# Kernel optimization log

Hardware: AMD Instinct MI355X
Metric: run time of the kernel (lower is better)

## Reference

```python
import jax, jax.numpy as jnp
import numpy as np

B, H, W, C = 1, 72, 72, 768
NH, HD = 12, 64
FF = 3072
EPS = 1e-6
THETA = 10000.0
S = H * W


def _rope_tables():
    freqs = 1.0 / THETA ** (np.arange(0, HD, 4, dtype=np.float32) / HD)  # [16]
    t = np.arange(H, dtype=np.float32)
    fx = np.outer(t, freqs)  # [72,16]
    fy = np.outer(t, freqs)
    fx = np.tile(fx[:, None, :], (1, W, 1))  # [72,72,16]
    fy = np.tile(fy[None, :, :], (H, 1, 1))
    fxy = np.concatenate([fx, fy], axis=-1).reshape(S, -1)  # [5184,32]
    fxy = np.repeat(fxy, 2, axis=-1)  # [5184,64]
    return jnp.asarray(np.cos(fxy)), jnp.asarray(np.sin(fxy))


def _rotate_pairwise(x):
    x1 = x[..., ::2]
    x2 = x[..., 1::2]
    return jnp.stack([-x2, x1], axis=-1).reshape(x.shape)


def _layernorm(x, g, b):
    m = jnp.mean(x, axis=-1, keepdims=True)
    v = jnp.mean(jnp.square(x - m), axis=-1, keepdims=True)
    return (x - m) * jax.lax.rsqrt(v + EPS) * g + b


def setup_inputs() -> dict:
    key = jax.random.key(0)
    ks = jax.random.split(key, 12)
    s_c = 1.0 / np.sqrt(C)
    s_ff = 1.0 / np.sqrt(FF)
    d = {
        "hidden_states": jax.random.normal(ks[0], (B, H, W, C), jnp.float32),
        "wq": jax.random.normal(ks[1], (C, C), jnp.float32) * s_c,
        "bq": jnp.zeros((C,), jnp.float32),
        "wk": jax.random.normal(ks[2], (C, C), jnp.float32) * s_c,
        "bk": jnp.zeros((C,), jnp.float32),
        "wv": jax.random.normal(ks[3], (C, C), jnp.float32) * s_c,
        "bv": jnp.zeros((C,), jnp.float32),
        "wo": jax.random.normal(ks[4], (C, C), jnp.float32) * s_c,
        "bo": jnp.zeros((C,), jnp.float32),
        "g1": jnp.ones((C,), jnp.float32),
        "b1": jnp.zeros((C,), jnp.float32),
        "g2": jnp.ones((C,), jnp.float32),
        "b2": jnp.zeros((C,), jnp.float32),
        "w_fc1": jax.random.normal(ks[5], (C, FF), jnp.float32) * s_c,
        "b_fc1": jnp.zeros((FF,), jnp.float32),
        "w_fc2": jax.random.normal(ks[6], (FF, C), jnp.float32) * s_ff,
        "b_fc2": jnp.zeros((C,), jnp.float32),
        "ls1": jnp.full((C,), 1e-5, jnp.float32),
        "ls2": jnp.full((C,), 1e-5, jnp.float32),
    }
    return d


def reference(hidden_states, wq, bq, wk, bk, wv, bv, wo, bo, g1, b1, g2, b2,
              w_fc1, b_fc1, w_fc2, b_fc2, ls1, ls2):
    cos, sin = _rope_tables()  # [S, HD]
    cos = cos[None, None]  # [1,1,S,HD]
    sin = sin[None, None]

    residual = hidden_states
    x = hidden_states.reshape(B, S, C)
    x = _layernorm(x, g1, b1)

    # attention
    q = (x @ wq + bq).reshape(B, S, NH, HD).transpose(0, 2, 1, 3)
    k = (x @ wk + bk).reshape(B, S, NH, HD).transpose(0, 2, 1, 3)
    v = (x @ wv + bv).reshape(B, S, NH, HD).transpose(0, 2, 1, 3)
    q = q * cos + _rotate_pairwise(q) * sin
    k = k * cos + _rotate_pairwise(k) * sin
    scale = HD ** -0.5
    attn = jax.nn.softmax(jnp.einsum('bhqd,bhkd->bhqk', q, k) * scale, axis=-1)
    o = jnp.einsum('bhqk,bhkd->bhqd', attn, v)
    o = o.transpose(0, 2, 1, 3).reshape(B, S, C)
    o = o @ wo + bo
    o = o * ls1

    hs = residual + o.reshape(B, H, W, C)
    residual = hs
    x = _layernorm(hs.reshape(B, S, C), g2, b2)
    x = jax.nn.gelu(x @ w_fc1 + b_fc1, approximate=False)
    x = x @ w_fc2 + b_fc2
    x = x * ls2
    return residual + x.reshape(B, H, W, C)
```

## Files before the change

kernel.cpp:

```cpp
#include <hip/hip_runtime.h>

#define S_  5184
#define C_  768
#define NH_ 12
#define HD_ 64
#define FF_ 3072
#define WW_ 72

typedef __attribute__((ext_vector_type(8))) short bf16x8;
typedef __attribute__((ext_vector_type(4))) float f32x4;

__device__ __forceinline__ float bf2f(unsigned short u){
    unsigned int i = ((unsigned int)u) << 16; float f; __builtin_memcpy(&f,&i,4); return f;
}
__device__ __forceinline__ unsigned short f2bf(float f){
    unsigned int i; __builtin_memcpy(&i,&f,4);
    unsigned int r = (i + 0x7fffu + ((i>>16)&1u)) >> 16;
    return (unsigned short)r;
}
__device__ __forceinline__ float ldf(float v){ return v; }
__device__ __forceinline__ float ldf(unsigned short v){ return bf2f(v); }

__device__ __forceinline__ void gload16(const void* g, const void* l) {
    __builtin_amdgcn_global_load_lds((const __attribute__((address_space(1))) void*)g,
                                     (__attribute__((address_space(3))) void*)l, 16, 0, 0);
}
__device__ __forceinline__ unsigned int cvtpk(float lo, float hi){
    unsigned int r;
    asm volatile("v_cvt_pk_bf16_f32 %0, %1, %2" : "=v"(r) : "v"(lo), "v"(hi));
    return r;
}

template<typename TIN>
__global__ __launch_bounds__(256) void ln_k(const TIN* __restrict__ x,
                                            const float* __restrict__ g,
                                            const float* __restrict__ b,
                                            unsigned short* __restrict__ out)
{
    int row = blockIdx.x, tid = threadIdx.x;
    const TIN* xr = x + (size_t)row * C_;
    float v0 = ldf(xr[tid]), v1 = ldf(xr[tid+256]), v2 = ldf(xr[tid+512]);
    float s = v0+v1+v2, q = v0*v0+v1*v1+v2*v2;
    #pragma unroll
    for (int off=32; off; off>>=1){ s += __shfl_xor(s,off); q += __shfl_xor(q,off); }
    __shared__ float ss[4], qq[4], mshare[2];
    int lane = tid & 63, wv = tid >> 6;
    if (!lane){ ss[wv] = s; qq[wv] = q; }
    __syncthreads();
    if (!tid){
        float S2 = ss[0]+ss[1]+ss[2]+ss[3];
        float Q2 = qq[0]+qq[1]+qq[2]+qq[3];
        float mean = S2 * (1.f/C_);
        float var  = Q2 * (1.f/C_) - mean*mean;
        mshare[0] = mean; mshare[1] = rsqrtf(var + 1e-6f);
    }
    __syncthreads();
    float mean = mshare[0], inv = mshare[1];
    unsigned short* orow = out + (size_t)row * C_;
    orow[tid]     = f2bf((v0-mean)*inv*g[tid]     + b[tid]);
    orow[tid+256] = f2bf((v1-mean)*inv*g[tid+256] + b[tid+256]);
    orow[tid+512] = f2bf((v2-mean)*inv*g[tid+512] + b[tid+512]);
}

__global__ __launch_bounds__(256) void rope_k(unsigned short* __restrict__ q,
                                              unsigned short* __restrict__ k)
{
    int idx = blockIdx.x * 256 + threadIdx.x;
    if (idx >= S_*32) return;
    int s = idx >> 5, i = idx & 31;
    int hh = s / WW_, ww = s % WW_;
    int m = i & 15;
    float coord = (i < 16) ? (float)hh : (float)ww;
    float freq = powf(10000.0f, -(float)m / 16.0f);
    float a = coord * freq;
    float c = cosf(a), sn = sinf(a);
    const float QS = 0.18033688011112042f;
    #pragma unroll
    for (int h = 0; h < NH_; h++) {
        size_t base = (size_t)s*C_ + h*HD_ + 2*i;
        float x0 = bf2f(q[base]), x1 = bf2f(q[base+1]);
        q[base]   = f2bf((x0*c - x1*sn) * QS);
        q[base+1] = f2bf((x1*c + x0*sn) * QS);
        x0 = bf2f(k[base]); x1 = bf2f(k[base+1]);
        k[base]   = f2bf(x0*c - x1*sn);
        k[base+1] = f2bf(x1*c + x0*sn);
    }
}

__global__ __launch_bounds__(256) void transpose_all(const float* __restrict__ wq, unsigned short* __restrict__ wqT,
                                                     const float* __restrict__ wk, unsigned short* __restrict__ wkT,
                                                     const float* __restrict__ wv, unsigned short* __restrict__ wvT,
                                                     const float* __restrict__ wo, unsigned short* __restrict__ woT,
                                                     const float* __restrict__ wf1, unsigned short* __restrict__ wf1T,
                                                     const float* __restrict__ wf2, unsigned short* __restrict__ wf2T)
{
    __shared__ float t[32][33];
    int b = blockIdx.x;
    const float* W; unsigned short* WT; int K, N, tb;
    if      (b < 576)  { W = wq;  WT = wqT;  K = 768;  N = 768;  tb = b; }
    else if (b < 1152) { W = wk;  WT = wkT;  K = 768;  N = 768;  tb = b - 576; }
    else if (b < 1728) { W = wv;  WT = wvT;  K = 768;  N = 768;  tb = b - 1152; }
    else if (b < 2304) { W = wo;  WT = woT;  K = 768;  N = 768;  tb = b - 1728; }
    else if (b < 4608) { W = wf1; WT = wf1T; K = 768;  N = 3072; tb = b - 2304; }
    else               { W = wf2; WT = wf2T; K = 3072; N = 768;  tb = b - 4608; }
    int ntx = N / 32;
    int n0 = (tb % ntx) * 32, k0 = (tb / ntx) * 32;
    int tx = threadIdx.x & 31, ty = threadIdx.x >> 5;
    #pragma unroll
    for (int i = 0; i < 4; i++)
        t[ty + i*8][tx] = W[(size_t)(k0 + ty + i*8)*N + n0 + tx];
    __syncthreads();
    #pragma unroll
    for (int i = 0; i < 4; i++)
        WT[(size_t)(n0 + ty + i*8)*K + k0 + tx] = f2bf(t[tx][ty + i*8]);
}

template<int EPI, int NWC, int BK, int KK, int NN>
__global__ __launch_bounds__(256) void gemm_mfma(const unsigned short* __restrict__ A,
                                                 const unsigned short* __restrict__ BT,
                                                 const float* __restrict__ bias,
                                                 const float* __restrict__ biasB,
                                                 const float* __restrict__ biasC,
                                                 const float* __restrict__ scale,
                                                 const float* __restrict__ addend,
                                                 void* __restrict__ outp,
                                                 void* __restrict__ outp2)
{
    const int BN = 64*NWC;
    const int MI = (NWC == 2) ? 4 : 2;
    const int M = S_;
    __shared__ __align__(16) unsigned short As[2][128*BK];
    __shared__ __align__(16) unsigned short Bs[2][64*NWC*BK];
    int tid = threadIdx.x;
    int w = tid >> 6, lane = tid & 63, lq = lane & 15, lk = lane >> 4;
    int wr = (NWC == 2) ? (w >> 1) : w;
    int wc = (NWC == 2) ? (w & 1) : 0;

    int gx = gridDim.x;
    int nwg = gx * gridDim.y;
    int bid = blockIdx.y * gx + blockIdx.x;
    int xcd = bid & 7, idx = bid >> 3;
    int qq = nwg >> 3, rr = nwg & 7;
    int wg = (xcd < rr) ? (xcd*(qq+1) + idx) : (rr*(qq+1) + (xcd-rr)*qq + idx);
    int bm = (wg / gx) * 128, bn = (wg % gx) * BN;

    f32x4 acc[MI][4];
    #pragma unroll
    for (int i = 0; i < MI; i++)
        #pragma unroll
        for (int j = 0; j < 4; j++) acc[i][j] = 0;

    auto STAGE = [&](int buf, int kt) {
        #pragma unroll
        for (int u = 0; u < BK/16; u++) {
            int t = w*(BK/16) + u;
            int c = t*64 + lane;
            int kg = c >> 7, row = c & 127;
            int ra = bm + row; if (ra >= M) ra = M - 1;
            gload16(A + (size_t)ra*KK + kt*BK + kg*8, As[buf] + t*512);
        }
        #pragma unroll
        for (int u = 0; u < BK*NWC/32; u++) {
            int t = w*(BK*NWC/32) + u;
            int c = t*64 + lane;
            int kg = (NWC == 2) ? (c >> 7) : (c >> 6);
            int row = (NWC == 2) ? (c & 127) : (c & 63);
            gload16(BT + (size_t)(bn + row)*KK + kt*BK + kg*8, Bs[buf] + t*512);
        }
    };

    auto COMPUTE = [&](int buf) {
        #pragma unroll
        for (int kk = 0; kk < BK/32; kk++) {
            bf16x8 af[MI], bfr[4];
            #pragma unroll
            for (int mi = 0; mi < MI; mi++)
                af[mi] = *(const bf16x8*)(As[buf] + (kk*4 + lk)*1024 + (wr*MI*16 + mi*16 + lq)*8);
            #pragma unroll
            for (int ni = 0; ni < 4; ni++)
                bfr[ni] = *(const bf16x8*)(Bs[buf] + (kk*4 + lk)*BN*8 + (wc*64 + ni*16 + lq)*8);
            #pragma unroll
            for (int mi = 0; mi < MI; mi++)
                #pragma unroll
                for (int ni = 0; ni < 4; ni++)
                    acc[mi][ni] = __builtin_amdgcn_mfma_f32_16x16x32_bf16(af[mi], bfr[ni], acc[mi][ni], 0, 0, 0);
        }
    };

    const int nk = KK / BK;
    STAGE(0, 0);
    #pragma unroll 1
    for (int kt = 0; kt < nk; kt += 2) {
        __syncthreads();
        if (kt + 1 < nk) STAGE(1, kt + 1);
        COMPUTE(0);
        __syncthreads();
        if (kt + 2 < nk) STAGE(0, kt + 2);
        COMPUTE(1);
    }

    #pragma unroll
    for (int mi = 0; mi < MI; mi++) {
        #pragma unroll
        for (int ni = 0; ni < 4; ni++) {
            int n = bn + wc*64 + ni*16 + lq;
            int m0 = bm + wr*MI*16 + mi*16 + lk*4;
            if (EPI == 4) {
                if (n < 1536) {
                    const float* bb = (n < 768) ? bias : biasB;
                    int nn = (n < 768) ? n : (n - 768);
                    size_t base = (n < 768) ? 0 : ((size_t)S_ * 768);
                    #pragma unroll
                    for (int r = 0; r < 4; r++) {
                        int m = m0 + r;
                        if (m < M)
                            ((unsigned short*)outp)[base + (size_t)m*768 + nn] = f2bf(acc[mi][ni][r] + bb[nn]);
                    }
                } else {
                    if (m0 < M) {
                        float bv = biasC[n - 1536];
                        ushort4 pv;
                        pv.x = f2bf(acc[mi][ni][0] + bv);
                        pv.y = f2bf(acc[mi][ni][1] + bv);
                        pv.z = f2bf(acc[mi][ni][2] + bv);
                        pv.w = f2bf(acc[mi][ni][3] + bv);
                        *(ushort4*)((unsigned short*)outp2 + (size_t)(n - 1536)*S_ + m0) = pv;
                    }
                }
            } else {
                #pragma unroll
                for (int r = 0; r < 4; r++) {
                    int m = m0 + r;
                    if (m < M) {
                        float v = acc[mi][ni][r] + bias[n];
                        if (EPI == 1) {
                            v = 0.5f * v * (1.f + erff(v * 0.70710678f));
                            ((unsigned short*)outp)[(size_t)m*NN + n] = f2bf(v);
                        } else {
                            size_t o = (size_t)m*NN + n;
                            ((float*)outp)[o] = v*scale[n] + addend[o];
                        }
                    }
                }
            }
        }
    }
}

__global__ __launch_bounds__(256) void attn_mfma6(const unsigned short* __restrict__ Q,
                                                  const unsigned short* __restrict__ Kb,
                                                  const unsigned short* __restrict__ Vt,
                                                  unsigned short* __restrict__ O)
{
    __shared__ __align__(16) unsigned short Ks[2][4096];
    __shared__ __align__(16) unsigned short Vs[2][4096];
    int tid = threadIdx.x;
    int w = tid >> 6, lane = tid & 63, lq = lane & 15, lk = lane >> 4;
    int h = blockIdx.y;
    int q0 = blockIdx.x * 128 + w * 32;

    bf16x8 qf[2][2];
    #pragma unroll
    for (int qi = 0; qi < 2; qi++) {
        int qr = q0 + qi*16 + lq; if (qr >= S_) qr = S_ - 1;
        #pragma unroll
        for (int ks = 0; ks < 2; ks++)
            qf[qi][ks] = *(const bf16x8*)(Q + (size_t)qr*C_ + h*64 + ks*32 + lk*8);
    }

    union { bf16x8 v; unsigned int u[4]; } ones;
    ones.u[0] = 0x3F803F80u; ones.u[1] = 0x3F803F80u;
    ones.u[2] = 0x3F803F80u; ones.u[3] = 0x3F803F80u;

    f32x4 oacc[2][4];
    #pragma unroll
    for (int qi = 0; qi < 2; qi++)
        #pragma unroll
        for (int df = 0; df < 4; df++) oacc[qi][df] = 0;
    f32x4 lacc[2];
    lacc[0] = 0; lacc[1] = 0;

    auto STAGE = [&](int buf, int t) {
        int kv0 = t * 64;
        #pragma unroll
        for (int u = 0; u < 4; u++) {
            int tt = w*4 + u;
            if (tt < 8)
                gload16(Kb + (size_t)(kv0 + lane)*C_ + h*64 + tt*8, Ks[buf] + tt*512);
            else
                gload16(Vt + (size_t)(h*64 + lane)*S_ + kv0 + (tt-8)*8, Vs[buf] + (tt-8)*512);
        }
    };

    auto BODY = [&](int buf) {
        f32x4 s[2][4];
        #pragma unroll
        for (int qi = 0; qi < 2; qi++)
            #pragma unroll
            for (int nf = 0; nf < 4; nf++) s[qi][nf] = -8.0f;
        __builtin_amdgcn_s_setprio(1);
        #pragma unroll
        for (int ks = 0; ks < 2; ks++) {
            #pragma unroll
            for (int nf = 0; nf < 4; nf++) {
                bf16x8 kf = *(const bf16x8*)(Ks[buf] + (ks*4 + lk)*512 + (nf*16 + lq)*8);
                #pragma unroll
                for (int qi = 0; qi < 2; qi++)
                    s[qi][nf] = __builtin_amdgcn_mfma_f32_16x16x32_bf16(kf, qf[qi][ks], s[qi][nf], 0, 0, 0);
            }
        }
        __builtin_amdgcn_s_setprio(0);

        unsigned int pk[2][8];
        #pragma unroll
        for (int qi = 0; qi < 2; qi++) {
            #pragma unroll
            for (int nf = 0; nf < 4; nf++) {
                float p0 = exp2f(s[qi][nf][0]);
                float p1 = exp2f(s[qi][nf][1]);
                float p2 = exp2f(s[qi][nf][2]);
                float p3 = exp2f(s[qi][nf][3]);
                pk[qi][nf*2+0] = cvtpk(p0, p1);
                pk[qi][nf*2+1] = cvtpk(p2, p3);
            }
        }

        __builtin_amdgcn_s_setprio(1);
        #pragma unroll
        for (int ks = 0; ks < 2; ks++) {
            union { bf16x8 v; unsigned int u[4]; } pb[2];
            #pragma unroll
            for (int qi = 0; qi < 2; qi++) {
                pb[qi].u[0] = pk[qi][4*ks+0]; pb[qi].u[1] = pk[qi][4*ks+1];
                pb[qi].u[2] = pk[qi][4*ks+2]; pb[qi].u[3] = pk[qi][4*ks+3];
                lacc[qi] = __builtin_amdgcn_mfma_f32_16x16x32_bf16(ones.v, pb[qi].v, lacc[qi], 0, 0, 0);
            }
            #pragma unroll
            for (int df = 0; df < 4; df++) {
                int d = df*16 + lq;
                union { bf16x8 v; unsigned long long dd[2]; } va;
                va.dd[0] = *(const unsigned long long*)(Vs[buf] + (4*ks + (lk>>1))*512 + d*8 + (lk&1)*4);
                va.dd[1] = *(const unsigned long long*)(Vs[buf] + (4*ks + 2 + (lk>>1))*512 + d*8 + (lk&1)*4);
                #pragma unroll
                for (int qi = 0; qi < 2; qi++)
                    oacc[qi][df] = __builtin_amdgcn_mfma_f32_16x16x32_bf16(va.v, pb[qi].v, oacc[qi][df], 0, 0, 0);
            }
        }
        __builtin_amdgcn_s_setprio(0);
    };

    STAGE(0, 0);
    #pragma unroll 1
    for (int t = 0; t < 80; t += 2) {
        __syncthreads();
        STAGE(1, t + 1);
        BODY(0);
        __syncthreads();
        STAGE(0, t + 2);
        BODY(1);
    }
    __syncthreads();
    BODY(0);

    #pragma unroll
    for (int qi = 0; qi < 2; qi++) {
        int q = q0 + qi*16 + lq;
        if (q < S_) {
            float rl = 1.f / lacc[qi][0];
            #pragma unroll
            for (int df = 0; df < 4; df++) {
                ushort4 pv;
                pv.x = f2bf(oacc[qi][df][0] * rl);
                pv.y = f2bf(oacc[qi][df][1] * rl);
                pv.z = f2bf(oacc[qi][df][2] * rl);
                pv.w = f2bf(oacc[qi][df][3] * rl);
                *(ushort4*)(O + (size_t)q*C_ + h*64 + df*16 + lk*4) = pv;
            }
        }
    }
}

extern "C" void kernel_launch(void* const* d_in, const int* in_sizes, int n_in,
                              void* d_out, int out_size, void* d_ws, size_t ws_size,
                              hipStream_t stream)
{
    const float* hidden = (const float*)d_in[0];
    const float* wq  = (const float*)d_in[1];
    const float* bq  = (const float*)d_in[2];
    const float* wk  = (const float*)d_in[3];
    const float* bk  = (const float*)d_in[4];
    const float* wv  = (const float*)d_in[5];
    const float* bv  = (const float*)d_in[6];
    const float* wo  = (const float*)d_in[7];
    const float* bo  = (const float*)d_in[8];
    const float* g1  = (const float*)d_in[9];
    const float* b1  = (const float*)d_in[10];
    const float* g2  = (const float*)d_in[11];
    const float* b2  = (const float*)d_in[12];
    const float* wf1 = (const float*)d_in[13];
    const float* bf1 = (const float*)d_in[14];
    const float* wf2 = (const float*)d_in[15];
    const float* bf2_ = (const float*)d_in[16];
    const float* ls1 = (const float*)d_in[17];
    const float* ls2 = (const float*)d_in[18];

    char* ws = (char*)d_ws;
    size_t off = 0;
    auto alloc = [&](size_t bytes) { char* p = ws + off; off += (bytes + 255) & ~(size_t)255; return p; };

    float* res1          = (float*)alloc((size_t)S_*C_*4);
    unsigned short* lnb  = (unsigned short*)alloc((size_t)S_*C_*2);
    unsigned short* qb   = (unsigned short*)alloc((size_t)S_*C_*2);
    unsigned short* kb   = (unsigned short*)alloc((size_t)S_*C_*2);
    unsigned short* vtb  = (unsigned short*)alloc((size_t)S_*C_*2);
    unsigned short* ob   = (unsigned short*)alloc((size_t)S_*C_*2);
    unsigned short* fc1b = qb;
    unsigned short* wqT  = (unsigned short*)alloc((size_t)C_*C_*2);
    unsigned short* wkT  = (unsigned short*)alloc((size_t)C_*C_*2);
    unsigned short* wvT  = (unsigned short*)alloc((size_t)C_*C_*2);
    unsigned short* woT  = (unsigned short*)alloc((size_t)C_*C_*2);
    unsigned short* wf1T = (unsigned short*)alloc((size_t)C_*FF_*2);
    unsigned short* wf2T = (unsigned short*)alloc((size_t)C_*FF_*2);
    float* outb = (float*)d_out;

    hipLaunchKernelGGL(transpose_all, dim3(6912), dim3(256), 0, stream,
                       wq, wqT, wk, wkT, wv, wvT, wo, woT, wf1, wf1T, wf2, wf2T);
    hipLaunchKernelGGL(ln_k<float>, dim3(S_), dim3(256), 0, stream, hidden, g1, b1, lnb);
    hipLaunchKernelGGL((gemm_mfma<4,2,32,768,2304>), dim3(18, 41), dim3(256), 0, stream,
                       lnb, wqT, bq, bk, bv, (const float*)nullptr, (const float*)nullptr,
                       (void*)qb, (void*)vtb);
    hipLaunchKernelGGL(rope_k, dim3((S_*32 + 255)/256), dim3(256), 0, stream, qb, kb);
    hipLaunchKernelGGL(attn_mfma6, dim3((S_ + 127)/128, NH_), dim3(256), 0, stream,
                       qb, kb, vtb, ob);
    hipLaunchKernelGGL((gemm_mfma<2,1,64,768,768>), dim3(12, 41), dim3(256), 0, stream,
                       ob, woT, bo, (const float*)nullptr, (const float*)nullptr, ls1, hidden,
                       (void*)res1, (void*)nullptr);
    hipLaunchKernelGGL(ln_k<float>, dim3(S_), dim3(256), 0, stream, res1, g2, b2, lnb);
    hipLaunchKernelGGL((gemm_mfma<1,2,32,768,3072>), dim3(24, 41), dim3(256), 0, stream,
                       lnb, wf1T, bf1, (const float*)nullptr, (const float*)nullptr,
                       (const float*)nullptr, (const float*)nullptr,
                       (void*)fc1b, (void*)nullptr);
    hipLaunchKernelGGL((gemm_mfma<2,1,64,3072,768>), dim3(12, 41), dim3(256), 0, stream,
                       fc1b, wf2T, bf2_, (const float*)nullptr, (const float*)nullptr, ls2, res1,
                       (void*)outb, (void*)nullptr);
    (void)in_sizes; (void)n_in; (void)out_size; (void)ws_size;
}
```

Measured before the change: 471.9 us.

## Deepen GEMM pipeline to 4-buffer LDS ring with one barrier per k-step

The bf16 MFMA GEMM now keeps a four-slot LDS ring and prefetches two k-tiles ahead with direct global-to-LDS loads. Each k-step uses explicit vmcnt waits and a single barrier, replacing the old double-buffered loop that had two syncthreads per pair of tiles. MFMA bursts are wrapped in raised wave priority. BK is fixed at 32 and M/N/K become runtime arguments, which cuts the outer-loop unrolling and constant folding, and the extra buffers use more LDS per block, which may reduce occupancy.

```diff
diff --git a/kernel.cpp b/kernel.cpp
--- a/kernel.cpp
+++ b/kernel.cpp
@@ -29,6 +29,13 @@
     unsigned int r;
     asm volatile("v_cvt_pk_bf16_f32 %0, %1, %2" : "=v"(r) : "v"(lo), "v"(hi));
     return r;
+}
+template<int N> __device__ __forceinline__ void waitvm(){
+    if      constexpr (N >= 8) asm volatile("s_waitcnt vmcnt(8)" ::: "memory");
+    else if constexpr (N == 6) asm volatile("s_waitcnt vmcnt(6)" ::: "memory");
+    else if constexpr (N == 4) asm volatile("s_waitcnt vmcnt(4)" ::: "memory");
+    else if constexpr (N == 3) asm volatile("s_waitcnt vmcnt(3)" ::: "memory");
+    else                       asm volatile("s_waitcnt vmcnt(0)" ::: "memory");
 }
 
 template<typename TIN>
@@ -115,7 +122,7 @@
         WT[(size_t)(n0 + ty + i*8)*K + k0 + tx] = f2bf(t[tx][ty + i*8]);
 }
 
-template<int EPI, int NWC, int BK, int KK, int NN>
+template<int EPI, int NWC>
 __global__ __launch_bounds__(256) void gemm_mfma(const unsigned short* __restrict__ A,
                                                  const unsigned short* __restrict__ BT,
                                                  const float* __restrict__ bias,
@@ -124,13 +131,15 @@
                                                  const float* __restrict__ scale,
                                                  const float* __restrict__ addend,
                                                  void* __restrict__ outp,
-                                                 void* __restrict__ outp2)
-{
+                                                 void* __restrict__ outp2,
+                                                 int M, int N, int K)
+{
+    const int BK = 32;
     const int BN = 64*NWC;
     const int MI = (NWC == 2) ? 4 : 2;
-    const int M = S_;
-    __shared__ __align__(16) unsigned short As[2][128*BK];
-    __shared__ __align__(16) unsigned short Bs[2][64*NWC*BK];
+    const int L  = BK/16 + BK*NWC/32;
+    __shared__ __align__(16) unsigned short As[4][128*BK];
+    __shared__ __align__(16) unsigned short Bs[4][64*NWC*BK];
     int tid = threadIdx.x;
     int w = tid >> 6, lane = tid & 63, lq = lane & 15, lk = lane >> 4;
     int wr = (NWC == 2) ? (w >> 1) : w;
@@ -157,7 +166,7 @@
             int c = t*64 + lane;
             int kg = c >> 7, row = c & 127;
             int ra = bm + row; if (ra >= M) ra = M - 1;
-            gload16(A + (size_t)ra*KK + kt*BK + kg*8, As[buf] + t*512);
+            gload16(A + (size_t)ra*K + kt*BK + kg*8, As[buf] + t*512);
         }
         #pragma unroll
         for (int u = 0; u < BK*NWC/32; u++) {
@@ -165,38 +174,38 @@
             int c = t*64 + lane;
             int kg = (NWC == 2) ? (c >> 7) : (c >> 6);
             int row = (NWC == 2) ? (c & 127) : (c & 63);
-            gload16(BT + (size_t)(bn + row)*KK + kt*BK + kg*8, Bs[buf] + t*512);
+            gload16(BT + (size_t)(bn + row)*K + kt*BK + kg*8, Bs[buf] + t*512);
         }
     };
 
     auto COMPUTE = [&](int buf) {
-        #pragma unroll
-        for (int kk = 0; kk < BK/32; kk++) {
-            bf16x8 af[MI], bfr[4];
-            #pragma unroll
-            for (int mi = 0; mi < MI; mi++)
-                af[mi] = *(const bf16x8*)(As[buf] + (kk*4 + lk)*1024 + (wr*MI*16 + mi*16 + lq)*8);
+        bf16x8 af[MI], bfr[4];
+        #pragma unroll
+        for (int mi = 0; mi < MI; mi++)
+            af[mi] = *(const bf16x8*)(As[buf] + lk*1024 + (wr*MI*16 + mi*16 + lq)*8);
+        #pragma unroll
+        for (int ni = 0; ni < 4; ni++)
+            bfr[ni] = *(const bf16x8*)(Bs[buf] + lk*BN*8 + (wc*64 + ni*16 + lq)*8);
+        __builtin_amdgcn_s_setprio(1);
+        #pragma unroll
+        for (int mi = 0; mi < MI; mi++)
             #pragma unroll
             for (int ni = 0; ni < 4; ni++)
-                bfr[ni] = *(const bf16x8*)(Bs[buf] + (kk*4 + lk)*BN*8 + (wc*64 + ni*16 + lq)*8);
-            #pragma unroll
-            for (int mi = 0; mi < MI; mi++)
-                #pragma unroll
-                for (int ni = 0; ni < 4; ni++)
-                    acc[mi][ni] = __builtin_amdgcn_mfma_f32_16x16x32_bf16(af[mi], bfr[ni], acc[mi][ni], 0, 0, 0);
-        }
+                acc[mi][ni] = __builtin_amdgcn_mfma_f32_16x16x32_bf16(af[mi], bfr[ni], acc[mi][ni], 0, 0, 0);
+        __builtin_amdgcn_s_setprio(0);
     };
 
-    const int nk = KK / BK;
+    int nk = K / BK;
     STAGE(0, 0);
+    STAGE(1, 1);
     #pragma unroll 1
-    for (int kt = 0; kt < nk; kt += 2) {
-        __syncthreads();
-        if (kt + 1 < nk) STAGE(1, kt + 1);
-        COMPUTE(0);
-        __syncthreads();
-        if (kt + 2 < nk) STAGE(0, kt + 2);
-        COMPUTE(1);
+    for (int kt = 0; kt < nk; kt++) {
+        if (kt + 2 < nk)      { STAGE((kt + 2) & 3, kt + 2); waitvm<2*L>(); }
+        else if (kt + 1 < nk) { waitvm<L>(); }
+        else                  { waitvm<0>(); }
+        __builtin_amdgcn_s_barrier();
+        __builtin_amdgcn_sched_barrier(0);
+        COMPUTE(kt & 3);
     }
 
     #pragma unroll
@@ -235,9 +244,9 @@
                         float v = acc[mi][ni][r] + bias[n];
                         if (EPI == 1) {
                             v = 0.5f * v * (1.f + erff(v * 0.70710678f));
-                            ((unsigned short*)outp)[(size_t)m*NN + n] = f2bf(v);
+                            ((unsigned short*)outp)[(size_t)m*N + n] = f2bf(v);
                         } else {
-                            size_t o = (size_t)m*NN + n;
+                            size_t o = (size_t)m*N + n;
                             ((float*)outp)[o] = v*scale[n] + addend[o];
                         }
                     }
@@ -426,22 +435,22 @@
     hipLaunchKernelGGL(transpose_all, dim3(6912), dim3(256), 0, stream,
                        wq, wqT, wk, wkT, wv, wvT, wo, woT, wf1, wf1T, wf2, wf2T);
     hipLaunchKernelGGL(ln_k<float>, dim3(S_), dim3(256), 0, stream, hidden, g1, b1, lnb);
-    hipLaunchKernelGGL((gemm_mfma<4,2,32,768,2304>), dim3(18, 41), dim3(256), 0, stream,
+    hipLaunchKernelGGL((gemm_mfma<4,2>), dim3(2304/128, 41), dim3(256), 0, stream,
                        lnb, wqT, bq, bk, bv, (const float*)nullptr, (const float*)nullptr,
-                       (void*)qb, (void*)vtb);
+                       (void*)qb, (void*)vtb, S_, 2304, C_);
     hipLaunchKernelGGL(rope_k, dim3((S_*32 + 255)/256), dim3(256), 0, stream, qb, kb);
     hipLaunchKernelGGL(attn_mfma6, dim3((S_ + 127)/128, NH_), dim3(256), 0, stream,
                        qb, kb, vtb, ob);
-    hipLaunchKernelGGL((gemm_mfma<2,1,64,768,768>), dim3(12, 41), dim3(256), 0, stream,
+    hipLaunchKernelGGL((gemm_mfma<2,1>), dim3(C_/64, 41), dim3(256), 0, stream,
                        ob, woT, bo, (const float*)nullptr, (const float*)nullptr, ls1, hidden,
-                       (void*)res1, (void*)nullptr);
+                       (void*)res1, (void*)nullptr, S_, C_, C_);
     hipLaunchKernelGGL(ln_k<float>, dim3(S_), dim3(256), 0, stream, res1, g2, b2, lnb);
-    hipLaunchKernelGGL((gemm_mfma<1,2,32,768,3072>), dim3(24, 41), dim3(256), 0, stream,
+    hipLaunchKernelGGL((gemm_mfma<1,2>), dim3(FF_/128, 41), dim3(256), 0, stream,
                        lnb, wf1T, bf1, (const float*)nullptr, (const float*)nullptr,
                        (const float*)nullptr, (const float*)nullptr,
-                       (void*)fc1b, (void*)nullptr);
-    hipLaunchKernelGGL((gemm_mfma<2,1,64,3072,768>), dim3(12, 41), dim3(256), 0, stream,
+                       (void*)fc1b, (void*)nullptr, S_, FF_, C_);
+    hipLaunchKernelGGL((gemm_mfma<2,1>), dim3(C_/64, 41), dim3(256), 0, stream,
                        fc1b, wf2T, bf2_, (const float*)nullptr, (const float*)nullptr, ls2, res1,
-                       (void*)outb, (void*)nullptr);
+                       (void*)outb, (void*)nullptr, S_, C_, FF_);
     (void)in_sizes; (void)n_in; (void)out_size; (void)ws_size;
 }
```

Result: slower. 523.8 us (+11.0%).
